# Kernel tuning notes

Measured on AMD Instinct MI355X. Metric: run time of the kernel, lower is better.

## Reference

```python
import jax, jax.numpy as jnp
import numpy as np

HIDDEN = 128
EDGE = 64
EPS = 1e-5

def setup_inputs() -> dict:
    key = jax.random.key(0)
    ks = jax.random.split(key, 12)
    B, N, D = 8, 256, HIDDEN
    h = jax.random.normal(ks[0], (B, N, D), dtype=jnp.float32)
    edge_feats = jax.random.normal(ks[1], (B, N, N, 3), dtype=jnp.float32)
    adj_mask = jax.random.bernoulli(ks[2], 0.5, (B, N, N))
    s = lambda fan_in: 1.0 / np.sqrt(fan_in)
    W1 = jax.random.uniform(ks[3], (D + 3, EDGE), minval=-s(D + 3), maxval=s(D + 3))
    b1 = jnp.zeros((EDGE,), jnp.float32)
    W2 = jax.random.uniform(ks[4], (EDGE, D), minval=-s(EDGE), maxval=s(EDGE))
    b2 = jnp.zeros((D,), jnp.float32)
    U1 = jax.random.uniform(ks[5], (3 * D, D), minval=-s(3 * D), maxval=s(3 * D))
    b3 = jnp.zeros((D,), jnp.float32)
    U2 = jax.random.uniform(ks[6], (D, D), minval=-s(D), maxval=s(D))
    b4 = jnp.zeros((D,), jnp.float32)
    gamma = jnp.ones((D,), jnp.float32)
    beta = jnp.zeros((D,), jnp.float32)
    return {"h": h, "edge_feats": edge_feats, "adj_mask": adj_mask,
            "W1": W1, "b1": b1, "W2": W2, "b2": b2,
            "U1": U1, "b3": b3, "U2": U2, "b4": b4,
            "gamma": gamma, "beta": beta}

def reference(h, edge_feats, adj_mask, W1, b1, W2, b2, U1, b3, U2, b4, gamma, beta):
    B, N, D = h.shape
    # NOTE: torch does h.unsqueeze(2).expand(B,N,N,D): h_j[b,i,j,:] = h[b,i,:]
    h_j = jnp.broadcast_to(h[:, :, None, :], (B, N, N, D))
    gate_in = jnp.concatenate([h_j, edge_feats], axis=-1)          # (B,N,N,D+3)
    gates = jax.nn.sigmoid(jax.nn.relu(gate_in @ W1 + b1) @ W2 + b2)  # (B,N,N,D)
    mask_f = adj_mask.astype(h.dtype)[..., None]                    # (B,N,N,1)
    messages = gates * h_j * mask_f
    neighbor_count = jnp.clip(jnp.sum(mask_f, axis=2), 1.0)         # (B,N,1)
    agg_mean = jnp.sum(messages, axis=2) / neighbor_count           # (B,N,D)
    msgs_max = jnp.where(adj_mask[..., None], messages, -jnp.inf)
    agg_max = jnp.max(msgs_max, axis=2)
    agg_max = jnp.where(jnp.isinf(agg_max), 0.0, agg_max)
    upd_in = jnp.concatenate([h, agg_mean, agg_max], axis=-1)       # (B,N,3D)
    upd = jax.nn.relu(upd_in @ U1 + b3) @ U2 + b4
    x = h + upd
    mu = jnp.mean(x, axis=-1, keepdims=True)
    var = jnp.var(x, axis=-1, keepdims=True)
    return (x - mu) * jax.lax.rsqrt(var + EPS) * gamma + beta
```

## Files before the change

kernel.cpp:

```cpp
#include <hip/hip_runtime.h>
#include <hip/hip_bf16.h>
#include <math.h>

#define NN 256
#define DD 128
#define EE 64
#define APAD 392
#define RPAD 136

typedef __attribute__((ext_vector_type(8))) short short8;
typedef __attribute__((ext_vector_type(4))) float f32x4;

static __device__ __forceinline__ unsigned short f2bf(float f) {
    __hip_bfloat16 b = __float2bfloat16(f);
    return *reinterpret_cast<unsigned short*>(&b);
}

static __device__ __forceinline__ short8 ldb(const float* __restrict__ B, int kbase, int d) {
    unsigned short tmp[8];
    #pragma unroll
    for (int j = 0; j < 8; ++j) tmp[j] = f2bf(B[(kbase + j) * DD + d]);
    return *(const short8*)tmp;
}

static __device__ __forceinline__ float sigm(float l) {
    return __fdividef(1.f, 1.f + __expf(-l));
}

__global__ __launch_bounds__(256, 4)
void ecgc_gate(const float* __restrict__ h_g,
               const float* __restrict__ ef_g,
               const int*   __restrict__ mask_g,
               const float* __restrict__ W1_g,
               const float* __restrict__ b1_g,
               const float* __restrict__ W2_g,
               const float* __restrict__ b2_g,
               const float* __restrict__ U1_g,
               const float* __restrict__ U2_g,
               float*          __restrict__ aggf,
               unsigned short* __restrict__ u1t,
               unsigned short* __restrict__ u2t)
{
    const int bi   = blockIdx.x;
    const int t    = threadIdx.x;
    const int lane = t & 63;
    const int w    = t >> 6;
    const int m16  = lane & 15;
    const int quad = lane >> 4;

    __shared__ __align__(16) float sh_ef4[NN * 4];
    __shared__ __align__(16) float sh_q4[EE * 4];
    __shared__ float sh_basep[4 * EE];
    __shared__ float sh_w1e[3 * EE];
    __shared__ int   sh_jlist[NN], sh_wcnt[4], sh_cnt;

    if (t < 32) {
        const int flat = bi * 32 + t;
        if (flat < 384 * DD) {
            const int d = flat / 384, k = flat - d * 384;
            u1t[flat] = f2bf(U1_g[k * DD + d]);
        } else {
            const int f2 = flat - 384 * DD;
            const int d = f2 >> 7, k = f2 & 127;
            u2t[f2] = f2bf(U2_g[k * DD + d]);
        }
    }

    {
        const float* efr = ef_g + (size_t)bi * NN * 3;
        sh_ef4[t * 4 + 0] = efr[t * 3 + 0];
        sh_ef4[t * 4 + 1] = efr[t * 3 + 1];
        sh_ef4[t * 4 + 2] = efr[t * 3 + 2];
        sh_ef4[t * 4 + 3] = 0.f;
    }
    if (t < 192) sh_w1e[t] = W1_g[(DD + (t >> 6)) * EE + (t & 63)];

    const int mk = (mask_g[bi * NN + t] != 0) ? 1 : 0;
    const unsigned long long bal = __ballot(mk);
    if (lane == 0) sh_wcnt[w] = __popcll(bal);
    const int pre = __popcll(bal & ((1ull << lane) - 1ull));

    {
        const int e = t & 63;
        float acc = 0.f;
        #pragma unroll 8
        for (int d = w * 32; d < w * 32 + 32; ++d)
            acc = fmaf(h_g[bi * DD + d], W1_g[d * EE + e], acc);
        sh_basep[w * EE + e] = acc;
    }

    const int dstripe = w * 32;
    short8 bfrag[2][2];
    float  nb2[2];
    #pragma unroll
    for (int dt = 0; dt < 2; ++dt) {
        const int d = dstripe + 16 * dt + m16;
        nb2[dt] = b2_g[d];
        #pragma unroll
        for (int kh = 0; kh < 2; ++kh)
            bfrag[dt][kh] = ldb(W2_g, kh * 32 + quad * 8, d);
    }
    __syncthreads();

    {
        int wbase = 0;
        for (int ww = 0; ww < w; ++ww) wbase += sh_wcnt[ww];
        if (mk) sh_jlist[wbase + pre] = t;
        if (t == 0) sh_cnt = sh_wcnt[0] + sh_wcnt[1] + sh_wcnt[2] + sh_wcnt[3];
    }
    if (t < EE) {
        const float base = b1_g[t] + sh_basep[t] + sh_basep[EE + t] +
                           sh_basep[2 * EE + t] + sh_basep[3 * EE + t];
        sh_q4[t * 4 + 0] = base;
        sh_q4[t * 4 + 1] = sh_w1e[t];
        sh_q4[t * 4 + 2] = sh_w1e[EE + t];
        sh_q4[t * 4 + 3] = sh_w1e[2 * EE + t];
    }
    __syncthreads();

    f32x4 qa[8], qb[8];
    #pragma unroll
    for (int jj = 0; jj < 8; ++jj) {
        qa[jj] = *(const f32x4*)&sh_q4[(quad * 8 + jj) * 4];
        qb[jj] = *(const f32x4*)&sh_q4[(32 + quad * 8 + jj) * 4];
    }

    const int cnt = sh_cnt;
    const int njt = (cnt + 15) >> 4;

    float sum2[2] = {0.f, 0.f};
    float mxl[2]  = {-3.0e38f, -3.0e38f};
    float mnl[2]  = { 3.0e38f,  3.0e38f};

    for (int jt = 0; jt < njt; ++jt) {
        const int row = jt * 16 + m16;
        int jl = sh_jlist[row];
        jl = (row < cnt) ? jl : 0;
        const float4 efv = *(const float4*)&sh_ef4[jl * 4];

        union { short8 s; __hip_bfloat162 h2[4]; } ua, ub;
        #pragma unroll
        for (int p = 0; p < 4; ++p) {
            const f32x4 qa0 = qa[2 * p], qa1 = qa[2 * p + 1];
            const f32x4 qb0 = qb[2 * p], qb1 = qb[2 * p + 1];
            float2 va, vb;
            va.x = fmaxf(fmaf(efv.z, qa0[3], fmaf(efv.y, qa0[2], fmaf(efv.x, qa0[1], qa0[0]))), 0.f);
            va.y = fmaxf(fmaf(efv.z, qa1[3], fmaf(efv.y, qa1[2], fmaf(efv.x, qa1[1], qa1[0]))), 0.f);
            vb.x = fmaxf(fmaf(efv.z, qb0[3], fmaf(efv.y, qb0[2], fmaf(efv.x, qb0[1], qb0[0]))), 0.f);
            vb.y = fmaxf(fmaf(efv.z, qb1[3], fmaf(efv.y, qb1[2], fmaf(efv.x, qb1[1], qb1[0]))), 0.f);
            ua.h2[p] = __float22bfloat162_rn(va);
            ub.h2[p] = __float22bfloat162_rn(vb);
        }

        const bool tail = (jt == njt - 1) && (cnt & 15);
        #pragma unroll
        for (int dt = 0; dt < 2; ++dt) {
            f32x4 acc = {nb2[dt], nb2[dt], nb2[dt], nb2[dt]};
            acc = __builtin_amdgcn_mfma_f32_16x16x32_bf16(ua.s, bfrag[dt][0], acc, 0, 0, 0);
            acc = __builtin_amdgcn_mfma_f32_16x16x32_bf16(ub.s, bfrag[dt][1], acc, 0, 0, 0);
            if (!tail) {
                #pragma unroll
                for (int r = 0; r < 4; ++r) {
                    const float l = acc[r];
                    mxl[dt] = fmaxf(mxl[dt], l);
                    mnl[dt] = fminf(mnl[dt], l);
                    sum2[dt] += sigm(l);
                }
            } else {
                #pragma unroll
                for (int r = 0; r < 4; ++r) {
                    const bool v = (jt * 16 + quad * 4 + r) < cnt;
                    const float lx = v ? acc[r] : -3.0e38f;
                    const float ln = v ? acc[r] :  3.0e38f;
                    mxl[dt] = fmaxf(mxl[dt], lx);
                    mnl[dt] = fminf(mnl[dt], ln);
                    sum2[dt] += sigm(lx);
                }
            }
        }
    }

    #pragma unroll
    for (int dt = 0; dt < 2; ++dt) {
        float s = sum2[dt], M = mxl[dt], m2 = mnl[dt];
        s += __shfl_xor(s, 16, 64);  s += __shfl_xor(s, 32, 64);
        M  = fmaxf(M,  __shfl_xor(M, 16, 64));  M  = fmaxf(M,  __shfl_xor(M, 32, 64));
        m2 = fminf(m2, __shfl_xor(m2, 16, 64)); m2 = fminf(m2, __shfl_xor(m2, 32, 64));
        if (quad == 0) {
            const int d = dstripe + 16 * dt + m16;
            const float hd = h_g[bi * DD + d];
            float mean = 0.f, amax = 0.f;
            if (cnt > 0) {
                mean = hd * s * __fdividef(1.f, (float)cnt);
                amax = (hd >= 0.f) ? hd * sigm(M) : hd * sigm(m2);
            }
            aggf[bi * 256 + d]       = mean;
            aggf[bi * 256 + 128 + d] = amax;
        }
    }
}

__global__ __launch_bounds__(256, 2)
void ecgc_upd(const float* __restrict__ h_g,
              const float* __restrict__ aggf,
              const unsigned short* __restrict__ u1t,
              const unsigned short* __restrict__ u2t,
              const float* __restrict__ b3_g,
              const float* __restrict__ b4_g,
              const float* __restrict__ gam_g,
              const float* __restrict__ bet_g,
              float*       __restrict__ out_g)
{
    const int bi0  = blockIdx.x * 16;
    const int t    = threadIdx.x;
    const int lane = t & 63;
    const int w    = t >> 6;
    const int m16  = lane & 15;
    const int quad = lane >> 4;

    __shared__ __align__(16) unsigned short shA[16 * APAD];
    __shared__ __align__(16) unsigned short rbuf[16 * RPAD];
    __shared__ float sh_s[4 * 16], sh_s2[4 * 16], sh_mu[16], sh_rs[16];

    {
        const int row = t >> 4, q = t & 15;
        const float* hrow = h_g  + (size_t)(bi0 + row) * DD;
        const float* wrow = aggf + (size_t)(bi0 + row) * 256;
        unsigned short tmp[24];
        #pragma unroll
        for (int c = 0; c < 24; ++c) {
            const int col = q * 24 + c;
            float v;
            if (col < 128)      v = hrow[col];
            else if (col < 256) v = wrow[col - 128];
            else                v = wrow[col - 256 + 128];
            tmp[c] = f2bf(v);
        }
        #pragma unroll
        for (int s8 = 0; s8 < 3; ++s8)
            *(short8*)&shA[row * APAD + q * 24 + s8 * 8] = *(const short8*)&tmp[s8 * 8];
    }
    __syncthreads();

    const int dstripe = w * 32;

    f32x4 acc[2];
    #pragma unroll
    for (int dt = 0; dt < 2; ++dt) {
        const float bb = b3_g[dstripe + dt * 16 + m16];
        acc[dt] = (f32x4){bb, bb, bb, bb};
    }
    for (int kk = 0; kk < 12; ++kk) {
        const short8 a0 = *(const short8*)&shA[m16 * APAD + kk * 32 + quad * 8];
        #pragma unroll
        for (int dt = 0; dt < 2; ++dt) {
            const int d = dstripe + dt * 16 + m16;
            const short8 b = *(const short8*)&u1t[(size_t)d * 384 + kk * 32 + quad * 8];
            acc[dt] = __builtin_amdgcn_mfma_f32_16x16x32_bf16(a0, b, acc[dt], 0, 0, 0);
        }
    }

    #pragma unroll
    for (int dt = 0; dt < 2; ++dt) {
        const int d = dstripe + dt * 16 + m16;
        #pragma unroll
        for (int r = 0; r < 4; ++r) {
            const int ro = quad * 4 + r;
            rbuf[ro * RPAD + d] = f2bf(fmaxf(acc[dt][r], 0.f));
        }
    }
    __syncthreads();

    f32x4 acc2[2];
    #pragma unroll
    for (int dt = 0; dt < 2; ++dt) {
        const float bb = b4_g[dstripe + dt * 16 + m16];
        acc2[dt] = (f32x4){bb, bb, bb, bb};
    }
    for (int kk = 0; kk < 4; ++kk) {
        const short8 a0 = *(const short8*)&rbuf[m16 * RPAD + kk * 32 + quad * 8];
        #pragma unroll
        for (int dt = 0; dt < 2; ++dt) {
            const int d = dstripe + dt * 16 + m16;
            const short8 b = *(const short8*)&u2t[(size_t)d * 128 + kk * 32 + quad * 8];
            acc2[dt] = __builtin_amdgcn_mfma_f32_16x16x32_bf16(a0, b, acc2[dt], 0, 0, 0);
        }
    }

    float xv[2][4];
    #pragma unroll
    for (int dt = 0; dt < 2; ++dt) {
        const int d = dstripe + dt * 16 + m16;
        #pragma unroll
        for (int r = 0; r < 4; ++r) {
            const int ro = quad * 4 + r;
            xv[dt][r] = h_g[(size_t)(bi0 + ro) * DD + d] + acc2[dt][r];
        }
    }

    #pragma unroll
    for (int r = 0; r < 4; ++r) {
        float s  = xv[0][r] + xv[1][r];
        float s2 = xv[0][r] * xv[0][r] + xv[1][r] * xv[1][r];
        #pragma unroll
        for (int off = 1; off < 16; off <<= 1) {
            s  += __shfl_xor(s,  off, 64);
            s2 += __shfl_xor(s2, off, 64);
        }
        if (m16 == 0) {
            const int ro = quad * 4 + r;
            sh_s[w * 16 + ro]  = s;
            sh_s2[w * 16 + ro] = s2;
        }
    }
    __syncthreads();
    if (t < 16) {
        const float S  = sh_s[t]  + sh_s[16 + t]  + sh_s[32 + t]  + sh_s[48 + t];
        const float S2 = sh_s2[t] + sh_s2[16 + t] + sh_s2[32 + t] + sh_s2[48 + t];
        const float mu  = S * (1.f / 128.f);
        const float var = S2 * (1.f / 128.f) - mu * mu;
        sh_mu[t] = mu;
        sh_rs[t] = rsqrtf(var + 1e-5f);
    }
    __syncthreads();

    #pragma unroll
    for (int dt = 0; dt < 2; ++dt) {
        const int d = dstripe + dt * 16 + m16;
        const float ga = gam_g[d], be = bet_g[d];
        #pragma unroll
        for (int r = 0; r < 4; ++r) {
            const int ro = quad * 4 + r;
            out_g[(size_t)(bi0 + ro) * DD + d] =
                (xv[dt][r] - sh_mu[ro]) * sh_rs[ro] * ga + be;
        }
    }
}

extern "C" void kernel_launch(void* const* d_in, const int* in_sizes, int n_in,
                              void* d_out, int out_size, void* d_ws, size_t ws_size,
                              hipStream_t stream) {
    float* aggf = (float*)d_ws;
    unsigned short* u1t = (unsigned short*)((char*)d_ws + (size_t)2048 * 256 * 4);
    unsigned short* u2t = u1t + 384 * DD;
    ecgc_gate<<<8 * NN, 256, 0, stream>>>(
        (const float*)d_in[0],
        (const float*)d_in[1],
        (const int*)d_in[2],
        (const float*)d_in[3],
        (const float*)d_in[4],
        (const float*)d_in[5],
        (const float*)d_in[6],
        (const float*)d_in[7],
        (const float*)d_in[9],
        aggf, u1t, u2t);
    ecgc_upd<<<(8 * NN) / 16, 256, 0, stream>>>(
        (const float*)d_in[0],
        aggf, u1t, u2t,
        (const float*)d_in[8],
        (const float*)d_in[10],
        (const float*)d_in[11],
        (const float*)d_in[12],
        (float*)d_out);
}
```

Before: 122.6 us.

## Split gate work across waves by neighbor tiles and pre-pack W2 to bf16

A separate pack kernel now converts W2, U1 and U2 to transposed bf16, so the gate kernel no longer does strided fp32 loads and conversions of W2 per block. Each wave previously handled a 32-column stripe of the output over every neighbor tile. Now each wave covers all 128 columns over a quarter of the neighbor tiles, with half the W2 fragment held in registers and half read from padded LDS. Partial sums, mins and maxes are then combined across waves through shared memory. The cost is an extra kernel launch, more LDS and an extra barrier, and higher register pressure from the 8-way accumulators.

```diff
diff --git a/kernel.cpp b/kernel.cpp
--- a/kernel.cpp
+++ b/kernel.cpp
@@ -7,6 +7,7 @@
 #define EE 64
 #define APAD 392
 #define RPAD 136
+#define WPAD 72
 
 typedef __attribute__((ext_vector_type(8))) short short8;
 typedef __attribute__((ext_vector_type(4))) float f32x4;
@@ -16,15 +17,25 @@
     return *reinterpret_cast<unsigned short*>(&b);
 }
 
-static __device__ __forceinline__ short8 ldb(const float* __restrict__ B, int kbase, int d) {
-    unsigned short tmp[8];
-    #pragma unroll
-    for (int j = 0; j < 8; ++j) tmp[j] = f2bf(B[(kbase + j) * DD + d]);
-    return *(const short8*)tmp;
-}
-
-static __device__ __forceinline__ float sigm(float l) {
-    return __fdividef(1.f, 1.f + __expf(-l));
+__global__ __launch_bounds__(256)
+void ecgc_pack(const float* __restrict__ W2_g, const float* __restrict__ U1_g,
+               const float* __restrict__ U2_g,
+               unsigned short* __restrict__ w2t, unsigned short* __restrict__ u1t,
+               unsigned short* __restrict__ u2t)
+{
+    const int idx = blockIdx.x * 256 + threadIdx.x;
+    if (idx < 8192) {
+        const int d = idx >> 6, k = idx & 63;
+        w2t[idx] = f2bf(W2_g[k * DD + d]);
+    } else if (idx < 8192 + 49152) {
+        const int i = idx - 8192;
+        const int d = i / 384, k = i - d * 384;
+        u1t[i] = f2bf(U1_g[k * DD + d]);
+    } else {
+        const int i = idx - 57344;
+        const int d = i >> 7, k = i & 127;
+        u2t[i] = f2bf(U2_g[k * DD + d]);
+    }
 }
 
 __global__ __launch_bounds__(256, 4)
@@ -33,13 +44,9 @@
                const int*   __restrict__ mask_g,
                const float* __restrict__ W1_g,
                const float* __restrict__ b1_g,
-               const float* __restrict__ W2_g,
                const float* __restrict__ b2_g,
-               const float* __restrict__ U1_g,
-               const float* __restrict__ U2_g,
-               float*          __restrict__ aggf,
-               unsigned short* __restrict__ u1t,
-               unsigned short* __restrict__ u2t)
+               const unsigned short* __restrict__ w2t,
+               float* __restrict__ aggf)
 {
     const int bi   = blockIdx.x;
     const int t    = threadIdx.x;
@@ -48,23 +55,13 @@
     const int m16  = lane & 15;
     const int quad = lane >> 4;
 
+    __shared__ __align__(16) unsigned short shW2[DD * WPAD];
     __shared__ __align__(16) float sh_ef4[NN * 4];
-    __shared__ __align__(16) float sh_q4[EE * 4];
+    __shared__ __align__(16) float sh_qs[16 * 20];
     __shared__ float sh_basep[4 * EE];
     __shared__ float sh_w1e[3 * EE];
+    __shared__ float sh_ps[4 * DD], sh_pmn[4 * DD], sh_pmx[4 * DD];
     __shared__ int   sh_jlist[NN], sh_wcnt[4], sh_cnt;
-
-    if (t < 32) {
-        const int flat = bi * 32 + t;
-        if (flat < 384 * DD) {
-            const int d = flat / 384, k = flat - d * 384;
-            u1t[flat] = f2bf(U1_g[k * DD + d]);
-        } else {
-            const int f2 = flat - 384 * DD;
-            const int d = f2 >> 7, k = f2 & 127;
-            u2t[f2] = f2bf(U2_g[k * DD + d]);
-        }
-    }
 
     {
         const float* efr = ef_g + (size_t)bi * NN * 3;
@@ -74,6 +71,14 @@
         sh_ef4[t * 4 + 3] = 0.f;
     }
     if (t < 192) sh_w1e[t] = W1_g[(DD + (t >> 6)) * EE + (t & 63)];
+
+    {
+        const int d = t >> 1, half = t & 1;
+        #pragma unroll
+        for (int b = 0; b < 4; ++b)
+            *(short8*)&shW2[d * WPAD + half * 32 + b * 8] =
+                *(const short8*)&w2t[d * EE + half * 32 + b * 8];
+    }
 
     const int mk = (mask_g[bi * NN + t] != 0) ? 1 : 0;
     const unsigned long long bal = __ballot(mk);
@@ -89,16 +94,13 @@
         sh_basep[w * EE + e] = acc;
     }
 
-    const int dstripe = w * 32;
-    short8 bfrag[2][2];
-    float  nb2[2];
-    #pragma unroll
-    for (int dt = 0; dt < 2; ++dt) {
-        const int d = dstripe + 16 * dt + m16;
+    short8 bfrag0[8];
+    float  nb2[8];
+    #pragma unroll
+    for (int dt = 0; dt < 8; ++dt) {
+        const int d = dt * 16 + m16;
         nb2[dt] = b2_g[d];
-        #pragma unroll
-        for (int kh = 0; kh < 2; ++kh)
-            bfrag[dt][kh] = ldb(W2_g, kh * 32 + quad * 8, d);
+        bfrag0[dt] = *(const short8*)&w2t[d * EE + quad * 8];
     }
     __syncthreads();
 
@@ -111,92 +113,122 @@
     if (t < EE) {
         const float base = b1_g[t] + sh_basep[t] + sh_basep[EE + t] +
                            sh_basep[2 * EE + t] + sh_basep[3 * EE + t];
-        sh_q4[t * 4 + 0] = base;
-        sh_q4[t * 4 + 1] = sh_w1e[t];
-        sh_q4[t * 4 + 2] = sh_w1e[EE + t];
-        sh_q4[t * 4 + 3] = sh_w1e[2 * EE + t];
-    }
-    __syncthreads();
-
-    f32x4 qa[8], qb[8];
-    #pragma unroll
-    for (int jj = 0; jj < 8; ++jj) {
-        qa[jj] = *(const f32x4*)&sh_q4[(quad * 8 + jj) * 4];
-        qb[jj] = *(const f32x4*)&sh_q4[(32 + quad * 8 + jj) * 4];
-    }
+        const int g = t >> 2, x = t & 3;
+        sh_qs[g * 20 + x]      = base;
+        sh_qs[g * 20 + 4 + x]  = sh_w1e[t];
+        sh_qs[g * 20 + 8 + x]  = sh_w1e[EE + t];
+        sh_qs[g * 20 + 12 + x] = sh_w1e[2 * EE + t];
+    }
+    __syncthreads();
 
     const int cnt = sh_cnt;
     const int njt = (cnt + 15) >> 4;
-
-    float sum2[2] = {0.f, 0.f};
-    float mxl[2]  = {-3.0e38f, -3.0e38f};
-    float mnl[2]  = { 3.0e38f,  3.0e38f};
-
-    for (int jt = 0; jt < njt; ++jt) {
+    const int qt  = (njt + 3) >> 2;
+    const int jt0 = w * qt;
+    const int jt1 = min(njt, jt0 + qt);
+
+    float sum[8], mnl[8], mxl[8];
+    #pragma unroll
+    for (int dt = 0; dt < 8; ++dt) { sum[dt] = 0.f; mnl[dt] = 3.0e38f; mxl[dt] = -3.0e38f; }
+
+    for (int jt = jt0; jt < jt1; ++jt) {
         const int row = jt * 16 + m16;
         int jl = sh_jlist[row];
         jl = (row < cnt) ? jl : 0;
         const float4 efv = *(const float4*)&sh_ef4[jl * 4];
+        const float ex = efv.x, ey = efv.y, ez = efv.z;
 
         union { short8 s; __hip_bfloat162 h2[4]; } ua, ub;
         #pragma unroll
-        for (int p = 0; p < 4; ++p) {
-            const f32x4 qa0 = qa[2 * p], qa1 = qa[2 * p + 1];
-            const f32x4 qb0 = qb[2 * p], qb1 = qb[2 * p + 1];
-            float2 va, vb;
-            va.x = fmaxf(fmaf(efv.z, qa0[3], fmaf(efv.y, qa0[2], fmaf(efv.x, qa0[1], qa0[0]))), 0.f);
-            va.y = fmaxf(fmaf(efv.z, qa1[3], fmaf(efv.y, qa1[2], fmaf(efv.x, qa1[1], qa1[0]))), 0.f);
-            vb.x = fmaxf(fmaf(efv.z, qb0[3], fmaf(efv.y, qb0[2], fmaf(efv.x, qb0[1], qb0[0]))), 0.f);
-            vb.y = fmaxf(fmaf(efv.z, qb1[3], fmaf(efv.y, qb1[2], fmaf(efv.x, qb1[1], qb1[0]))), 0.f);
-            ua.h2[p] = __float22bfloat162_rn(va);
-            ub.h2[p] = __float22bfloat162_rn(vb);
+        for (int p = 0; p < 2; ++p) {
+            {
+                const float* q = &sh_qs[(quad * 2 + p) * 20];
+                const f32x4 bs = *(const f32x4*)q;
+                const f32x4 w0 = *(const f32x4*)(q + 4);
+                const f32x4 w1 = *(const f32x4*)(q + 8);
+                const f32x4 w2 = *(const f32x4*)(q + 12);
+                float2 r0, r1;
+                r0.x = fmaxf(fmaf(ez, w2[0], fmaf(ey, w1[0], fmaf(ex, w0[0], bs[0]))), 0.f);
+                r0.y = fmaxf(fmaf(ez, w2[1], fmaf(ey, w1[1], fmaf(ex, w0[1], bs[1]))), 0.f);
+                r1.x = fmaxf(fmaf(ez, w2[2], fmaf(ey, w1[2], fmaf(ex, w0[2], bs[2]))), 0.f);
+                r1.y = fmaxf(fmaf(ez, w2[3], fmaf(ey, w1[3], fmaf(ex, w0[3], bs[3]))), 0.f);
+                ua.h2[2 * p]     = __float22bfloat162_rn(r0);
+                ua.h2[2 * p + 1] = __float22bfloat162_rn(r1);
+            }
+            {
+                const float* q = &sh_qs[(8 + quad * 2 + p) * 20];
+                const f32x4 bs = *(const f32x4*)q;
+                const f32x4 w0 = *(const f32x4*)(q + 4);
+                const f32x4 w1 = *(const f32x4*)(q + 8);
+                const f32x4 w2 = *(const f32x4*)(q + 12);
+                float2 r0, r1;
+                r0.x = fmaxf(fmaf(ez, w2[0], fmaf(ey, w1[0], fmaf(ex, w0[0], bs[0]))), 0.f);
+                r0.y = fmaxf(fmaf(ez, w2[1], fmaf(ey, w1[1], fmaf(ex, w0[1], bs[1]))), 0.f);
+                r1.x = fmaxf(fmaf(ez, w2[2], fmaf(ey, w1[2], fmaf(ex, w0[2], bs[2]))), 0.f);
+                r1.y = fmaxf(fmaf(ez, w2[3], fmaf(ey, w1[3], fmaf(ex, w0[3], bs[3]))), 0.f);
+                ub.h2[2 * p]     = __float22bfloat162_rn(r0);
+                ub.h2[2 * p + 1] = __float22bfloat162_rn(r1);
+            }
         }
 
         const bool tail = (jt == njt - 1) && (cnt & 15);
         #pragma unroll
-        for (int dt = 0; dt < 2; ++dt) {
+        for (int dt = 0; dt < 8; ++dt) {
+            const short8 b1f = *(const short8*)&shW2[(dt * 16 + m16) * WPAD + 32 + quad * 8];
             f32x4 acc = {nb2[dt], nb2[dt], nb2[dt], nb2[dt]};
-            acc = __builtin_amdgcn_mfma_f32_16x16x32_bf16(ua.s, bfrag[dt][0], acc, 0, 0, 0);
-            acc = __builtin_amdgcn_mfma_f32_16x16x32_bf16(ub.s, bfrag[dt][1], acc, 0, 0, 0);
+            acc = __builtin_amdgcn_mfma_f32_16x16x32_bf16(ua.s, bfrag0[dt], acc, 0, 0, 0);
+            acc = __builtin_amdgcn_mfma_f32_16x16x32_bf16(ub.s, b1f,        acc, 0, 0, 0);
             if (!tail) {
                 #pragma unroll
                 for (int r = 0; r < 4; ++r) {
                     const float l = acc[r];
                     mxl[dt] = fmaxf(mxl[dt], l);
                     mnl[dt] = fminf(mnl[dt], l);
-                    sum2[dt] += sigm(l);
+                    sum[dt] += __fdividef(1.f, 1.f + __expf(-l));
                 }
             } else {
                 #pragma unroll
                 for (int r = 0; r < 4; ++r) {
                     const bool v = (jt * 16 + quad * 4 + r) < cnt;
-                    const float lx = v ? acc[r] : -3.0e38f;
+                    const float lp = v ? acc[r] : -3.0e38f;
                     const float ln = v ? acc[r] :  3.0e38f;
-                    mxl[dt] = fmaxf(mxl[dt], lx);
+                    mxl[dt] = fmaxf(mxl[dt], lp);
                     mnl[dt] = fminf(mnl[dt], ln);
-                    sum2[dt] += sigm(lx);
+                    sum[dt] += __fdividef(1.f, 1.f + __expf(-lp));
                 }
             }
         }
     }
 
     #pragma unroll
-    for (int dt = 0; dt < 2; ++dt) {
-        float s = sum2[dt], M = mxl[dt], m2 = mnl[dt];
+    for (int dt = 0; dt < 8; ++dt) {
+        float s = sum[dt], mn = mnl[dt], mx = mxl[dt];
         s += __shfl_xor(s, 16, 64);  s += __shfl_xor(s, 32, 64);
-        M  = fmaxf(M,  __shfl_xor(M, 16, 64));  M  = fmaxf(M,  __shfl_xor(M, 32, 64));
-        m2 = fminf(m2, __shfl_xor(m2, 16, 64)); m2 = fminf(m2, __shfl_xor(m2, 32, 64));
+        mn = fminf(mn, __shfl_xor(mn, 16, 64)); mn = fminf(mn, __shfl_xor(mn, 32, 64));
+        mx = fmaxf(mx, __shfl_xor(mx, 16, 64)); mx = fmaxf(mx, __shfl_xor(mx, 32, 64));
         if (quad == 0) {
-            const int d = dstripe + 16 * dt + m16;
-            const float hd = h_g[bi * DD + d];
-            float mean = 0.f, amax = 0.f;
-            if (cnt > 0) {
-                mean = hd * s * __fdividef(1.f, (float)cnt);
-                amax = (hd >= 0.f) ? hd * sigm(M) : hd * sigm(m2);
-            }
-            aggf[bi * 256 + d]       = mean;
-            aggf[bi * 256 + 128 + d] = amax;
-        }
+            const int d = dt * 16 + m16;
+            sh_ps[w * DD + d]  = s;
+            sh_pmn[w * DD + d] = mn;
+            sh_pmx[w * DD + d] = mx;
+        }
+    }
+    __syncthreads();
+
+    if (t < DD) {
+        const float s = sh_ps[t] + sh_ps[DD + t] + sh_ps[2 * DD + t] + sh_ps[3 * DD + t];
+        float mn = fminf(fminf(sh_pmn[t], sh_pmn[DD + t]), fminf(sh_pmn[2 * DD + t], sh_pmn[3 * DD + t]));
+        float mx = fmaxf(fmaxf(sh_pmx[t], sh_pmx[DD + t]), fmaxf(sh_pmx[2 * DD + t], sh_pmx[3 * DD + t]));
+        const float hd = h_g[bi * DD + t];
+        float mean = 0.f, amax = 0.f;
+        if (cnt > 0) {
+            mean = hd * s * __fdividef(1.f, (float)cnt);
+            const float gmax = __fdividef(1.f, 1.f + __expf(-mx));
+            const float gmin = __fdividef(1.f, 1.f + __expf(-mn));
+            amax = (hd >= 0.f) ? hd * gmax : hd * gmin;
+        }
+        aggf[bi * 256 + t]       = mean;
+        aggf[bi * 256 + 128 + t] = amax;
     }
 }
 
@@ -343,17 +375,20 @@
     float* aggf = (float*)d_ws;
     unsigned short* u1t = (unsigned short*)((char*)d_ws + (size_t)2048 * 256 * 4);
     unsigned short* u2t = u1t + 384 * DD;
+    unsigned short* w2t = u2t + 128 * DD;
+    ecgc_pack<<<288, 256, 0, stream>>>(
+        (const float*)d_in[5],
+        (const float*)d_in[7],
+        (const float*)d_in[9],
+        w2t, u1t, u2t);
     ecgc_gate<<<8 * NN, 256, 0, stream>>>(
         (const float*)d_in[0],
         (const float*)d_in[1],
         (const int*)d_in[2],
         (const float*)d_in[3],
         (const float*)d_in[4],
-        (const float*)d_in[5],
         (const float*)d_in[6],
-        (const float*)d_in[7],
-        (const float*)d_in[9],
-        aggf, u1t, u2t);
+        w2t, aggf);
     ecgc_upd<<<(8 * NN) / 16, 256, 0, stream>>>(
         (const float*)d_in[0],
         aggf, u1t, u2t,
```

Result: slower. 313.3 us (+155.6%).

## Split gate-kernel waves over neighbor halves and wider D stripes

Applied to the files above, without the earlier changes.

Work in the gate kernel is repartitioned. Each wave now covers half the neighbor tiles and 64 output features (four MFMA column tiles), where before it covered every neighbor tile and 32 features. Partial sum, max and min go through shared memory and are combined after an extra barrier. The per-tile ReLU layer-1 projection is now computed once per 64 features instead of once per 32, which halves that redundant work. The first-layer coefficients are read from shared memory inside the loop instead of being held in registers, trading register pressure for extra LDS reads.

```diff
diff --git a/kernel.cpp b/kernel.cpp
--- a/kernel.cpp
+++ b/kernel.cpp
@@ -16,15 +16,15 @@
     return *reinterpret_cast<unsigned short*>(&b);
 }
 
+static __device__ __forceinline__ float sigm(float l) {
+    return __fdividef(1.f, 1.f + __expf(-l));
+}
+
 static __device__ __forceinline__ short8 ldb(const float* __restrict__ B, int kbase, int d) {
     unsigned short tmp[8];
     #pragma unroll
     for (int j = 0; j < 8; ++j) tmp[j] = f2bf(B[(kbase + j) * DD + d]);
     return *(const short8*)tmp;
-}
-
-static __device__ __forceinline__ float sigm(float l) {
-    return __fdividef(1.f, 1.f + __expf(-l));
 }
 
 __global__ __launch_bounds__(256, 4)
@@ -47,11 +47,14 @@
     const int w    = t >> 6;
     const int m16  = lane & 15;
     const int quad = lane >> 4;
+    const int jh   = w >> 1;
+    const int dh   = w & 1;
 
     __shared__ __align__(16) float sh_ef4[NN * 4];
-    __shared__ __align__(16) float sh_q4[EE * 4];
+    __shared__ __align__(16) float sh_qs[16 * 20];
     __shared__ float sh_basep[4 * EE];
     __shared__ float sh_w1e[3 * EE];
+    __shared__ float sh_ps[2 * DD], sh_pmx[2 * DD], sh_pmn[2 * DD];
     __shared__ int   sh_jlist[NN], sh_wcnt[4], sh_cnt;
 
     if (t < 32) {
@@ -60,9 +63,9 @@
             const int d = flat / 384, k = flat - d * 384;
             u1t[flat] = f2bf(U1_g[k * DD + d]);
         } else {
-            const int f2 = flat - 384 * DD;
-            const int d = f2 >> 7, k = f2 & 127;
-            u2t[f2] = f2bf(U2_g[k * DD + d]);
+            const int f2i = flat - 384 * DD;
+            const int d = f2i >> 7, k = f2i & 127;
+            u2t[f2i] = f2bf(U2_g[k * DD + d]);
         }
     }
 
@@ -89,12 +92,11 @@
         sh_basep[w * EE + e] = acc;
     }
 
-    const int dstripe = w * 32;
-    short8 bfrag[2][2];
-    float  nb2[2];
-    #pragma unroll
-    for (int dt = 0; dt < 2; ++dt) {
-        const int d = dstripe + 16 * dt + m16;
+    short8 bfrag[4][2];
+    float  nb2[4];
+    #pragma unroll
+    for (int dt = 0; dt < 4; ++dt) {
+        const int d = dh * 64 + dt * 16 + m16;
         nb2[dt] = b2_g[d];
         #pragma unroll
         for (int kh = 0; kh < 2; ++kh)
@@ -111,50 +113,67 @@
     if (t < EE) {
         const float base = b1_g[t] + sh_basep[t] + sh_basep[EE + t] +
                            sh_basep[2 * EE + t] + sh_basep[3 * EE + t];
-        sh_q4[t * 4 + 0] = base;
-        sh_q4[t * 4 + 1] = sh_w1e[t];
-        sh_q4[t * 4 + 2] = sh_w1e[EE + t];
-        sh_q4[t * 4 + 3] = sh_w1e[2 * EE + t];
-    }
-    __syncthreads();
-
-    f32x4 qa[8], qb[8];
-    #pragma unroll
-    for (int jj = 0; jj < 8; ++jj) {
-        qa[jj] = *(const f32x4*)&sh_q4[(quad * 8 + jj) * 4];
-        qb[jj] = *(const f32x4*)&sh_q4[(32 + quad * 8 + jj) * 4];
-    }
+        const int g = t >> 2, x = t & 3;
+        sh_qs[g * 20 + x]      = base;
+        sh_qs[g * 20 + 4 + x]  = sh_w1e[t];
+        sh_qs[g * 20 + 8 + x]  = sh_w1e[EE + t];
+        sh_qs[g * 20 + 12 + x] = sh_w1e[2 * EE + t];
+    }
+    __syncthreads();
 
     const int cnt = sh_cnt;
     const int njt = (cnt + 15) >> 4;
-
-    float sum2[2] = {0.f, 0.f};
-    float mxl[2]  = {-3.0e38f, -3.0e38f};
-    float mnl[2]  = { 3.0e38f,  3.0e38f};
-
-    for (int jt = 0; jt < njt; ++jt) {
+    const int hjt = (njt + 1) >> 1;
+    const int jt0 = jh * hjt;
+    const int jt1 = min(njt, jt0 + hjt);
+
+    float sum[4], mxl[4], mnl[4];
+    #pragma unroll
+    for (int dt = 0; dt < 4; ++dt) { sum[dt] = 0.f; mxl[dt] = -3.0e38f; mnl[dt] = 3.0e38f; }
+
+    for (int jt = jt0; jt < jt1; ++jt) {
         const int row = jt * 16 + m16;
         int jl = sh_jlist[row];
         jl = (row < cnt) ? jl : 0;
         const float4 efv = *(const float4*)&sh_ef4[jl * 4];
+        const float ex = efv.x, ey = efv.y, ez = efv.z;
 
         union { short8 s; __hip_bfloat162 h2[4]; } ua, ub;
         #pragma unroll
-        for (int p = 0; p < 4; ++p) {
-            const f32x4 qa0 = qa[2 * p], qa1 = qa[2 * p + 1];
-            const f32x4 qb0 = qb[2 * p], qb1 = qb[2 * p + 1];
-            float2 va, vb;
-            va.x = fmaxf(fmaf(efv.z, qa0[3], fmaf(efv.y, qa0[2], fmaf(efv.x, qa0[1], qa0[0]))), 0.f);
-            va.y = fmaxf(fmaf(efv.z, qa1[3], fmaf(efv.y, qa1[2], fmaf(efv.x, qa1[1], qa1[0]))), 0.f);
-            vb.x = fmaxf(fmaf(efv.z, qb0[3], fmaf(efv.y, qb0[2], fmaf(efv.x, qb0[1], qb0[0]))), 0.f);
-            vb.y = fmaxf(fmaf(efv.z, qb1[3], fmaf(efv.y, qb1[2], fmaf(efv.x, qb1[1], qb1[0]))), 0.f);
-            ua.h2[p] = __float22bfloat162_rn(va);
-            ub.h2[p] = __float22bfloat162_rn(vb);
+        for (int g2 = 0; g2 < 2; ++g2) {
+            {
+                const float* q = &sh_qs[(quad * 2 + g2) * 20];
+                const f32x4 bs = *(const f32x4*)q;
+                const f32x4 w0 = *(const f32x4*)(q + 4);
+                const f32x4 w1 = *(const f32x4*)(q + 8);
+                const f32x4 w2 = *(const f32x4*)(q + 12);
+                float2 r0, r1;
+                r0.x = fmaxf(fmaf(ez, w2[0], fmaf(ey, w1[0], fmaf(ex, w0[0], bs[0]))), 0.f);
+                r0.y = fmaxf(fmaf(ez, w2[1], fmaf(ey, w1[1], fmaf(ex, w0[1], bs[1]))), 0.f);
+                r1.x = fmaxf(fmaf(ez, w2[2], fmaf(ey, w1[2], fmaf(ex, w0[2], bs[2]))), 0.f);
+                r1.y = fmaxf(fmaf(ez, w2[3], fmaf(ey, w1[3], fmaf(ex, w0[3], bs[3]))), 0.f);
+                ua.h2[2 * g2]     = __float22bfloat162_rn(r0);
+                ua.h2[2 * g2 + 1] = __float22bfloat162_rn(r1);
+            }
+            {
+                const float* q = &sh_qs[(8 + quad * 2 + g2) * 20];
+                const f32x4 bs = *(const f32x4*)q;
+                const f32x4 w0 = *(const f32x4*)(q + 4);
+                const f32x4 w1 = *(const f32x4*)(q + 8);
+                const f32x4 w2 = *(const f32x4*)(q + 12);
+                float2 r0, r1;
+                r0.x = fmaxf(fmaf(ez, w2[0], fmaf(ey, w1[0], fmaf(ex, w0[0], bs[0]))), 0.f);
+                r0.y = fmaxf(fmaf(ez, w2[1], fmaf(ey, w1[1], fmaf(ex, w0[1], bs[1]))), 0.f);
+                r1.x = fmaxf(fmaf(ez, w2[2], fmaf(ey, w1[2], fmaf(ex, w0[2], bs[2]))), 0.f);
+                r1.y = fmaxf(fmaf(ez, w2[3], fmaf(ey, w1[3], fmaf(ex, w0[3], bs[3]))), 0.f);
+                ub.h2[2 * g2]     = __float22bfloat162_rn(r0);
+                ub.h2[2 * g2 + 1] = __float22bfloat162_rn(r1);
+            }
         }
 
         const bool tail = (jt == njt - 1) && (cnt & 15);
         #pragma unroll
-        for (int dt = 0; dt < 2; ++dt) {
+        for (int dt = 0; dt < 4; ++dt) {
             f32x4 acc = {nb2[dt], nb2[dt], nb2[dt], nb2[dt]};
             acc = __builtin_amdgcn_mfma_f32_16x16x32_bf16(ua.s, bfrag[dt][0], acc, 0, 0, 0);
             acc = __builtin_amdgcn_mfma_f32_16x16x32_bf16(ub.s, bfrag[dt][1], acc, 0, 0, 0);
@@ -164,7 +183,7 @@
                     const float l = acc[r];
                     mxl[dt] = fmaxf(mxl[dt], l);
                     mnl[dt] = fminf(mnl[dt], l);
-                    sum2[dt] += sigm(l);
+                    sum[dt] += sigm(l);
                 }
             } else {
                 #pragma unroll
@@ -174,29 +193,39 @@
                     const float ln = v ? acc[r] :  3.0e38f;
                     mxl[dt] = fmaxf(mxl[dt], lx);
                     mnl[dt] = fminf(mnl[dt], ln);
-                    sum2[dt] += sigm(lx);
+                    sum[dt] += sigm(lx);
                 }
             }
         }
     }
 
     #pragma unroll
-    for (int dt = 0; dt < 2; ++dt) {
-        float s = sum2[dt], M = mxl[dt], m2 = mnl[dt];
+    for (int dt = 0; dt < 4; ++dt) {
+        float s = sum[dt], M = mxl[dt], m2 = mnl[dt];
         s += __shfl_xor(s, 16, 64);  s += __shfl_xor(s, 32, 64);
         M  = fmaxf(M,  __shfl_xor(M, 16, 64));  M  = fmaxf(M,  __shfl_xor(M, 32, 64));
         m2 = fminf(m2, __shfl_xor(m2, 16, 64)); m2 = fminf(m2, __shfl_xor(m2, 32, 64));
         if (quad == 0) {
-            const int d = dstripe + 16 * dt + m16;
-            const float hd = h_g[bi * DD + d];
-            float mean = 0.f, amax = 0.f;
-            if (cnt > 0) {
-                mean = hd * s * __fdividef(1.f, (float)cnt);
-                amax = (hd >= 0.f) ? hd * sigm(M) : hd * sigm(m2);
-            }
-            aggf[bi * 256 + d]       = mean;
-            aggf[bi * 256 + 128 + d] = amax;
-        }
+            const int d = dh * 64 + dt * 16 + m16;
+            sh_ps[jh * DD + d]  = s;
+            sh_pmx[jh * DD + d] = M;
+            sh_pmn[jh * DD + d] = m2;
+        }
+    }
+    __syncthreads();
+
+    if (t < DD) {
+        const float s  = sh_ps[t] + sh_ps[DD + t];
+        const float mx = fmaxf(sh_pmx[t], sh_pmx[DD + t]);
+        const float mn = fminf(sh_pmn[t], sh_pmn[DD + t]);
+        const float hd = h_g[bi * DD + t];
+        float mean = 0.f, amax = 0.f;
+        if (cnt > 0) {
+            mean = hd * s * __fdividef(1.f, (float)cnt);
+            amax = (hd >= 0.f) ? hd * sigm(mx) : hd * sigm(mn);
+        }
+        aggf[bi * 256 + t]       = mean;
+        aggf[bi * 256 + 128 + t] = amax;
     }
 }
 
```

Result: slower. 151.5 us (+23.6%).
